# Optimization experiments

Measured on AMD Instinct MI355X. Metric: run time of the kernel, lower is better.

The kernel has to match this reference:

```python
import jax, jax.numpy as jnp
import numpy as np


def setup_inputs() -> dict:
    key = jax.random.key(0)
    target = jax.random.normal(key, (32, 4, 512), dtype=jnp.float32)
    return {"target": target}


def reference(target):
    # target: [B, T, N] float32
    B, T, N = target.shape
    y = jnp.fft.fft(target)  # [B, T, N] complex64
    k = jnp.arange(N)
    # circulant(roll(y,-1))[k, l] == y[(l - k) mod N]
    idx = (k[None, :] - k[:, None]) % N  # [N, N] int
    C = y[..., idx]                      # [B, T, N, N]
    # Bx[k, l] = y[k] * conj(y[l]) * y[(l - k) mod N]
    Bx = y[..., :, None] * jnp.conj(y)[..., None, :] * C  # [B, T, N, N]
    # stack real/imag as channels, average over targets_count
    source = jnp.stack([Bx.real, Bx.imag], axis=2).mean(axis=1)  # [B, 2, N, N]
    return source, target
```

## Files before the change

### kernel.cpp

```cpp
#include <hip/hip_runtime.h>
#include <math.h>


#define NN 512
#define TT 4
#define BB 32

__global__ __launch_bounds__(256) void dft_kernel(const float* __restrict__ x,
                                                  float2* __restrict__ y,
                                                  float* __restrict__ tail) {
    __shared__ float2 part[128];

    int bt = blockIdx.x >> 2;
    int kq = blockIdx.x & 3;
    int kl = threadIdx.x & 127;
    int nh = threadIdx.x >> 7;
    int k  = (kq << 7) | kl;
    const float* xp = x + (size_t)bt * NN;

    if (kq == 0 && nh == 0) {
        ((float4*)(tail + (size_t)bt * NN))[kl] = ((const float4*)xp)[kl];
    }

    int n0 = nh << 8;
    const float twopi_n = -2.0f * (float)M_PI / (float)NN;

    float2 w0, w1, w2, w3;
    float s4, c4;
    {
        int m0 = (k * (n0 + 0)) & (NN - 1);
        int m1 = (k * (n0 + 1)) & (NN - 1);
        int m2 = (k * (n0 + 2)) & (NN - 1);
        int m3 = (k * (n0 + 3)) & (NN - 1);
        int m4 = (k * 4) & (NN - 1);
        sincosf(twopi_n * (float)m0, &w0.y, &w0.x);
        sincosf(twopi_n * (float)m1, &w1.y, &w1.x);
        sincosf(twopi_n * (float)m2, &w2.y, &w2.x);
        sincosf(twopi_n * (float)m3, &w3.y, &w3.x);
        sincosf(twopi_n * (float)m4, &s4, &c4);
    }

    float2 a0 = make_float2(0.f, 0.f), a1 = a0, a2 = a0, a3 = a0;

    #pragma unroll 4
    for (int n = n0; n < n0 + 256; n += 4) {
        float x0 = xp[n];
        float x1 = xp[n + 1];
        float x2 = xp[n + 2];
        float x3 = xp[n + 3];
        a0.x += x0 * w0.x; a0.y += x0 * w0.y;
        a1.x += x1 * w1.x; a1.y += x1 * w1.y;
        a2.x += x2 * w2.x; a2.y += x2 * w2.y;
        a3.x += x3 * w3.x; a3.y += x3 * w3.y;
        float t;
        t = w0.x * c4 - w0.y * s4; w0.y = w0.x * s4 + w0.y * c4; w0.x = t;
        t = w1.x * c4 - w1.y * s4; w1.y = w1.x * s4 + w1.y * c4; w1.x = t;
        t = w2.x * c4 - w2.y * s4; w2.y = w2.x * s4 + w2.y * c4; w2.x = t;
        t = w3.x * c4 - w3.y * s4; w3.y = w3.x * s4 + w3.y * c4; w3.x = t;
    }

    float re = (a0.x + a1.x) + (a2.x + a3.x);
    float im = (a0.y + a1.y) + (a2.y + a3.y);

    if (nh == 1) {
        part[kl] = make_float2(re, im);
    }
    __syncthreads();
    if (nh == 0) {
        float2 p = part[kl];
        y[(size_t)bt * NN + k] = make_float2(re + p.x, im + p.y);
    }
}

__global__ __launch_bounds__(256) void bispec_kernel(const float2* __restrict__ y,
                                                     float* __restrict__ out) {
    __shared__ float2 ring[TT * 2 * NN];

    int b     = blockIdx.x >> 6;
    int kbase = (blockIdx.x & 63) << 3;
    int tid   = threadIdx.x;

    const float4* src = (const float4*)(y + (size_t)b * TT * NN);
    float4* dst4 = (float4*)ring;
    #pragma unroll
    for (int i = 0; i < 4; ++i) {
        int g = tid + 256 * i;
        int t = g >> 8;
        int j = g & 255;
        float4 v = src[g];
        dst4[(t << 9) + j]       = v;
        dst4[(t << 9) + j + 256] = v;
    }
    __syncthreads();

    int l0 = tid;

    float2 b0[TT], b1[TT];
    #pragma unroll
    for (int t = 0; t < TT; ++t) {
        b0[t] = ring[(t << 10) + l0];
        b1[t] = ring[(t << 10) + l0 + 256];
    }

    float r0[8], i0[8], r1[8], i1[8];
    #pragma unroll
    for (int kk = 0; kk < 8; ++kk) { r0[kk] = i0[kk] = r1[kk] = i1[kk] = 0.f; }

    int w0base = (l0 - kbase - 7) & (NN - 1);
    int w1base = (l0 + 256 - kbase - 7) & (NN - 1);

    #pragma unroll
    for (int t = 0; t < TT; ++t) {
        const float2* rt = ring + (t << 10);
        float2 cw0[8], cw1[8], av[8];
        #pragma unroll
        for (int j = 0; j < 8; ++j) {
            cw0[j] = rt[w0base + j];
            cw1[j] = rt[w1base + j];
            av[j]  = rt[kbase + j];
        }
        #pragma unroll
        for (int kk = 0; kk < 8; ++kk) {
            float2 a  = av[kk];
            float2 c0 = cw0[7 - kk];
            float2 c1 = cw1[7 - kk];
            float ur0 = a.x * c0.x - a.y * c0.y;
            float ui0 = a.x * c0.y + a.y * c0.x;
            r0[kk] += ur0 * b0[t].x + ui0 * b0[t].y;
            i0[kk] += ui0 * b0[t].x - ur0 * b0[t].y;
            float ur1 = a.x * c1.x - a.y * c1.y;
            float ui1 = a.x * c1.y + a.y * c1.x;
            r1[kk] += ur1 * b1[t].x + ui1 * b1[t].y;
            i1[kk] += ui1 * b1[t].x - ur1 * b1[t].y;
        }
    }

    float* outb = out + (size_t)b * 2 * NN * NN;
    #pragma unroll
    for (int kk = 0; kk < 8; ++kk) {
        size_t rk = (size_t)(kbase + kk) * NN + l0;
        outb[rk]                 = r0[kk] * 0.25f;
        outb[rk + 256]           = r1[kk] * 0.25f;
        outb[NN * NN + rk]       = i0[kk] * 0.25f;
        outb[NN * NN + rk + 256] = i1[kk] * 0.25f;
    }
}

extern "C" void kernel_launch(void* const* d_in, const int* in_sizes, int n_in,
                              void* d_out, int out_size, void* d_ws, size_t ws_size,
                              hipStream_t stream) {
    const float* target = (const float*)d_in[0];
    float* out = (float*)d_out;
    float2* y = (float2*)d_ws;
    float* tail = out + (size_t)BB * 2 * NN * NN;

    dft_kernel<<<BB * TT * 4, 256, 0, stream>>>(target, y, tail);
    bispec_kernel<<<BB * 64, 256, 0, stream>>>(y, out);
}
```

Before: 93.25 us.

## Retile bispectrum kernel to 4x4 register blocks with swizzled LDS and float4 stores

Each thread in the bispectrum kernel now computes a 4x4 tile: 4 rows k by 4 consecutive columns l. Before, it computed 8 rows by 2 strided columns. The shared-memory ring is stored with an XOR-free index swizzle so that strided float2 reads by neighbouring threads avoid bank conflicts. Outputs are written as float4 vectors instead of scalar stores. The aim is to cut LDS reads per FMA and make the global stores, which dominate this write-bound kernel, wider. The cost is more index arithmetic and a scattered LDS fill.

Result: faster. 91.01 us (-2.4%).

```diff
diff --git a/kernel.cpp b/kernel.cpp
--- a/kernel.cpp
+++ b/kernel.cpp
@@ -5,6 +5,10 @@
 #define NN 512
 #define TT 4
 #define BB 32
+
+__device__ __forceinline__ int sw_idx(int idx) {
+    return (idx & ~63) | ((idx & 3) << 4) | ((idx >> 2) & 15);
+}
 
 __global__ __launch_bounds__(256) void dft_kernel(const float* __restrict__ x,
                                                   float2* __restrict__ y,
@@ -76,73 +80,79 @@
                                                      float* __restrict__ out) {
     __shared__ float2 ring[TT * 2 * NN];
 
-    int b     = blockIdx.x >> 6;
-    int kbase = (blockIdx.x & 63) << 3;
-    int tid   = threadIdx.x;
+    int b   = blockIdx.x >> 6;
+    int kb  = blockIdx.x & 63;
+    int tid = threadIdx.x;
 
     const float4* src = (const float4*)(y + (size_t)b * TT * NN);
-    float4* dst4 = (float4*)ring;
     #pragma unroll
     for (int i = 0; i < 4; ++i) {
         int g = tid + 256 * i;
         int t = g >> 8;
         int j = g & 255;
         float4 v = src[g];
-        dst4[(t << 9) + j]       = v;
-        dst4[(t << 9) + j + 256] = v;
+        int s0 = sw_idx((t << 10) + 2 * j);
+        ring[s0]       = make_float2(v.x, v.y);
+        ring[s0 + 16]  = make_float2(v.z, v.w);
+        ring[s0 + 512] = make_float2(v.x, v.y);
+        ring[s0 + 528] = make_float2(v.z, v.w);
     }
     __syncthreads();
 
-    int l0 = tid;
+    int kg    = tid >> 7;
+    int ll    = tid & 127;
+    int l0    = ll << 2;
+    int kbase = (kb << 3) | (kg << 2);
 
-    float2 b0[TT], b1[TT];
+    int w0 = (l0 - kbase - 3) & (NN - 1);
+    int swj[7];
     #pragma unroll
-    for (int t = 0; t < TT; ++t) {
-        b0[t] = ring[(t << 10) + l0];
-        b1[t] = ring[(t << 10) + l0 + 256];
-    }
+    for (int j = 0; j < 7; ++j) swj[j] = sw_idx(w0 + j);
+    int sa = sw_idx(kbase);
+    int sb = sw_idx(l0);
 
-    float r0[8], i0[8], r1[8], i1[8];
+    float r[4][4], q[4][4];
     #pragma unroll
-    for (int kk = 0; kk < 8; ++kk) { r0[kk] = i0[kk] = r1[kk] = i1[kk] = 0.f; }
-
-    int w0base = (l0 - kbase - 7) & (NN - 1);
-    int w1base = (l0 + 256 - kbase - 7) & (NN - 1);
+    for (int kk = 0; kk < 4; ++kk)
+        #pragma unroll
+        for (int c = 0; c < 4; ++c) { r[kk][c] = 0.f; q[kk][c] = 0.f; }
 
     #pragma unroll
     for (int t = 0; t < TT; ++t) {
         const float2* rt = ring + (t << 10);
-        float2 cw0[8], cw1[8], av[8];
+        float2 cw[7], av[4], bb[4];
         #pragma unroll
-        for (int j = 0; j < 8; ++j) {
-            cw0[j] = rt[w0base + j];
-            cw1[j] = rt[w1base + j];
-            av[j]  = rt[kbase + j];
-        }
+        for (int j = 0; j < 7; ++j) cw[j] = rt[swj[j]];
         #pragma unroll
-        for (int kk = 0; kk < 8; ++kk) {
-            float2 a  = av[kk];
-            float2 c0 = cw0[7 - kk];
-            float2 c1 = cw1[7 - kk];
-            float ur0 = a.x * c0.x - a.y * c0.y;
-            float ui0 = a.x * c0.y + a.y * c0.x;
-            r0[kk] += ur0 * b0[t].x + ui0 * b0[t].y;
-            i0[kk] += ui0 * b0[t].x - ur0 * b0[t].y;
-            float ur1 = a.x * c1.x - a.y * c1.y;
-            float ui1 = a.x * c1.y + a.y * c1.x;
-            r1[kk] += ur1 * b1[t].x + ui1 * b1[t].y;
-            i1[kk] += ui1 * b1[t].x - ur1 * b1[t].y;
+        for (int kk = 0; kk < 4; ++kk) av[kk] = rt[sa + (kk << 4)];
+        #pragma unroll
+        for (int c = 0; c < 4; ++c)  bb[c]  = rt[sb + (c << 4)];
+
+        #pragma unroll
+        for (int kk = 0; kk < 4; ++kk) {
+            float2 a = av[kk];
+            #pragma unroll
+            for (int c = 0; c < 4; ++c) {
+                float2 cv = cw[3 - kk + c];
+                float2 bv = bb[c];
+                float ur = a.x * cv.x - a.y * cv.y;
+                float ui = a.x * cv.y + a.y * cv.x;
+                r[kk][c] += ur * bv.x + ui * bv.y;
+                q[kk][c] += ui * bv.x - ur * bv.y;
+            }
         }
     }
 
     float* outb = out + (size_t)b * 2 * NN * NN;
     #pragma unroll
-    for (int kk = 0; kk < 8; ++kk) {
+    for (int kk = 0; kk < 4; ++kk) {
         size_t rk = (size_t)(kbase + kk) * NN + l0;
-        outb[rk]                 = r0[kk] * 0.25f;
-        outb[rk + 256]           = r1[kk] * 0.25f;
-        outb[NN * NN + rk]       = i0[kk] * 0.25f;
-        outb[NN * NN + rk + 256] = i1[kk] * 0.25f;
+        float4 vr = make_float4(r[kk][0] * 0.25f, r[kk][1] * 0.25f,
+                                r[kk][2] * 0.25f, r[kk][3] * 0.25f);
+        float4 vq = make_float4(q[kk][0] * 0.25f, q[kk][1] * 0.25f,
+                                q[kk][2] * 0.25f, q[kk][3] * 0.25f);
+        *(float4*)(outb + rk)                    = vr;
+        *(float4*)(outb + (size_t)NN * NN + rk)  = vq;
     }
 }
 
```
